# Performance work log

Hardware: AMD Instinct MI355X
Metric: run time of the kernel (lower is better)

Reference implementation:

```python
import jax, jax.numpy as jnp
import numpy as np

NUM_HEADS = 16

def setup_inputs() -> dict:
    key = jax.random.key(0)
    k1, k2, k3 = jax.random.split(key, 3)
    B, T, D = 4, 2048, 1024
    x = jax.random.normal(k1, (B, T, D), dtype=jnp.float32)
    # lecun_normal: std = 1/sqrt(fan_in)
    w = jax.random.normal(k2, (3 * D, D), dtype=jnp.float32) * (1.0 / np.sqrt(D))
    w_out = jax.random.normal(k3, (D, D), dtype=jnp.float32) * (1.0 / np.sqrt(D))
    return {"x": x, "w": w, "w_out": w_out}


def reference(x, w, w_out):
    B, T, D = x.shape
    H = NUM_HEADS
    L = D // H
    # qkv projection: (B,T,3D)
    q, k, v = jnp.split(jnp.matmul(x, w.T), 3, axis=2)
    # -> (T,B,H,L) time-major for the scan
    q = q.reshape(B, T, H, L).transpose(1, 0, 2, 3)
    k = k.reshape(B, T, H, L).transpose(1, 0, 2, 3)
    v = v.reshape(B, T, H, L).transpose(1, 0, 2, 3)
    scale = jax.lax.rsqrt(jnp.float32(L))
    k_exp = jnp.exp(k * scale) + 1e-6            # (T,B,H,L)
    k_norm = jnp.cumsum(k_exp, axis=0)           # causal normalizer
    qs = jax.nn.softmax(q * scale, axis=-1) / k_norm

    def step(carry, args):
        qs_t, k_t, v_t = args                    # each (B,H,L)
        # accumulate outer product k_t v_t^T into (B,H,L,L) state
        carry = carry + k_t[..., :, None] * v_t[..., None, :]
        y_t = jnp.einsum('bhl,bhlm->bhm', qs_t, carry)
        return carry, y_t

    init = jnp.zeros((B, H, L, L), dtype=x.dtype)
    _, y = jax.lax.scan(step, init, (qs, k_exp, v))   # y: (T,B,H,L)
    y = y.reshape(T, B, D).transpose(1, 0, 2)         # (B,T,D)
    return jnp.matmul(y, w_out)                       # Dense, no bias
```

## Files before the change

kernel.cpp:

```cpp
#include <hip/hip_runtime.h>
#include <math.h>

#define Bsz   4
#define Tsz   2048
#define Dsz   1024
#define Hsz   16
#define Lsz   64
#define BHsz  64
#define CH    64
#define NCH   32
#define QKVLD 3072
#define SCL   0.125f
#define QSC   512.0f
#define QSCI  (1.0f/512.0f)

typedef float  floatx4 __attribute__((ext_vector_type(4)));
typedef _Float16 half8 __attribute__((ext_vector_type(8)));
typedef _Float16 half4 __attribute__((ext_vector_type(4)));
typedef _Float16 half2v __attribute__((ext_vector_type(2)));

#define AS1 __attribute__((address_space(1)))
#define AS3 __attribute__((address_space(3)))

static __device__ __forceinline__ void gload_lds16(const void* g, void* l) {
  __builtin_amdgcn_global_load_lds((const AS1 unsigned int*)g,
                                   (AS3 unsigned int*)l, 16, 0, 0);
}

static __device__ __forceinline__ float wave_max64(float v) {
#pragma unroll
  for (int off = 1; off < 64; off <<= 1) v = fmaxf(v, __shfl_xor(v, off));
  return v;
}
static __device__ __forceinline__ float wave_sum64(float v) {
#pragma unroll
  for (int off = 1; off < 64; off <<= 1) v += __shfl_xor(v, off);
  return v;
}

__launch_bounds__(256)
__global__ void prep(const float* __restrict__ x, _Float16* __restrict__ xh,
                     const float* __restrict__ w, _Float16* __restrict__ wh,
                     const float* __restrict__ wo, _Float16* __restrict__ woT) {
  const int blk = blockIdx.x, tid = threadIdx.x;
  if (blk < 11264) {
    const float* in  = (blk < 8192) ? x : w;
    _Float16*   outp = (blk < 8192) ? xh : wh;
    const int bi = (blk < 8192) ? blk : blk - 8192;
    const int i = (bi * 256 + tid) * 4;
    float4 v = *(const float4*)(in + i);
    half4 h = { (_Float16)v.x, (_Float16)v.y, (_Float16)v.z, (_Float16)v.w };
    *(half4*)(outp + i) = h;
  } else {
    __shared__ float tile[32][33];
    const int bi = blk - 11264;
    const int bx = (bi & 31) * 32;
    const int by = (bi >> 5) * 32;
    const int tx = tid & 31, ty0 = tid >> 5;
#pragma unroll
    for (int p = 0; p < 4; p++) {
      const int ty = ty0 + p * 8;
      tile[ty][tx] = wo[(size_t)(by + ty) * 1024 + bx + tx];
    }
    __syncthreads();
#pragma unroll
    for (int p = 0; p < 4; p++) {
      const int ty = ty0 + p * 8;
      woT[(size_t)(bx + ty) * 1024 + by + tx] = (_Float16)tile[tx][ty];
    }
  }
}

__launch_bounds__(512, 2)
__global__ void qkv_gemm8(const _Float16* __restrict__ A, const _Float16* __restrict__ B,
                          _Float16* __restrict__ C) {
  __shared__ __align__(16) _Float16 AsF[2 * 256 * 64];
  __shared__ __align__(16) _Float16 BsF[2 * 256 * 64];
  const int tid  = threadIdx.x;
  const int wv   = tid >> 6, lane = tid & 63;
  const int wm   = wv >> 2, wn = wv & 3;
  const int fr   = lane & 15, fq = lane >> 4;

  const int flat = blockIdx.x;
  const int g  = (flat & 7) * 48 + (flat >> 3);
  const int m0 = (g / 12) * 256;
  const int n0 = (g % 12) * 256;

  const int srow = lane >> 3;
  const int scg  = (lane & 7) ^ srow;
  const int wv8  = wv * 8;
  const _Float16* aSrc = A + (size_t)(m0 + wv8 + srow) * 1024 + scg * 8;
  const _Float16* bSrc = B + (size_t)(n0 + wv8 + srow) * 1024 + scg * 8;

  const int sw  = fr & 7;
  const int ck0 = ((0 + fq) ^ sw) * 8;
  const int ck1 = ((4 + fq) ^ sw) * 8;
  const _Float16* apt = AsF + (wm * 64 + fr) * 64;
  const _Float16* bpt = BsF + (wn * 32 + fr) * 64;

  floatx4 acc[8][4];
#pragma unroll
  for (int i = 0; i < 8; i++)
#pragma unroll
    for (int j = 0; j < 4; j++) acc[i][j] = (floatx4){0.f, 0.f, 0.f, 0.f};

  half8 aF[8];
  half8 bF0[4], bF1[4];

#define BAR2() do { __builtin_amdgcn_s_barrier();                              \
                    asm volatile("" ::: "memory"); } while (0)
#define VMW4() asm volatile("s_waitcnt vmcnt(4)" ::: "memory")
#define SYNC() do { __builtin_amdgcn_s_barrier();                              \
    asm volatile("s_waitcnt lgkmcnt(0)" ::: "memory");                         \
    __builtin_amdgcn_sched_barrier(0); } while (0)

#define STAGE_A(kt, hm, sbuf) do {                                             \
    const _Float16* s_ = aSrc + (hm) * (128 * 1024) + (kt) * 64;               \
    gload_lds16(s_,             &AsF[(sbuf) * 16384 + ((hm) * 128 + wv8) * 64]);      \
    gload_lds16(s_ + 64 * 1024, &AsF[(sbuf) * 16384 + ((hm) * 128 + 64 + wv8) * 64]); \
  } while (0)
#define STAGE_B(kt, hm, sbuf) do {                                             \
    const _Float16* s_ = bSrc + (hm) * (128 * 1024) + (kt) * 64;               \
    gload_lds16(s_,             &BsF[(sbuf) * 16384 + ((hm) * 128 + wv8) * 64]);      \
    gload_lds16(s_ + 64 * 1024, &BsF[(sbuf) * 16384 + ((hm) * 128 + 64 + wv8) * 64]); \
  } while (0)

#define RD_A(buf, qm) do {                                                     \
    _Pragma("unroll")                                                          \
    for (int mf = 0; mf < 4; mf++) {                                           \
      const _Float16* p_ = apt + (buf) * 16384 + (qm) * 8192 + mf * 1024;      \
      aF[mf * 2]     = *(const half8*)(p_ + ck0);                              \
      aF[mf * 2 + 1] = *(const half8*)(p_ + ck1);                              \
    } } while (0)
#define RD_B(buf, qn, dst) do {                                                \
    _Pragma("unroll")                                                          \
    for (int nf = 0; nf < 2; nf++) {                                           \
      const _Float16* p_ = bpt + (buf) * 16384 + (qn) * 8192 + nf * 1024;      \
      dst[nf * 2]     = *(const half8*)(p_ + ck0);                             \
      dst[nf * 2 + 1] = *(const half8*)(p_ + ck1);                             \
    } } while (0)

#define MM(qm, qn, bb) do {                                                    \
    __builtin_amdgcn_s_setprio(1);                                             \
    _Pragma("unroll")                                                          \
    for (int mf = 0; mf < 4; mf++)                                             \
      _Pragma("unroll")                                                        \
      for (int nf = 0; nf < 2; nf++) {                                         \
        acc[(qm) * 4 + mf][(qn) * 2 + nf] = __builtin_amdgcn_mfma_f32_16x16x32_f16( \
            aF[mf * 2], bb[nf * 2], acc[(qm) * 4 + mf][(qn) * 2 + nf], 0, 0, 0);     \
        acc[(qm) * 4 + mf][(qn) * 2 + nf] = __builtin_amdgcn_mfma_f32_16x16x32_f16( \
            aF[mf * 2 + 1], bb[nf * 2 + 1], acc[(qm) * 4 + mf][(qn) * 2 + nf], 0, 0, 0); \
      }                                                                        \
    __builtin_amdgcn_s_setprio(0);                                             \
  } while (0)

  STAGE_A(0, 0, 0); STAGE_B(0, 0, 0); STAGE_A(0, 1, 0); STAGE_B(0, 1, 0);
  STAGE_A(1, 0, 1); STAGE_B(1, 0, 1);
  VMW4(); BAR2();

#pragma unroll 1
  for (int t = 0; t < 16; t += 2) {
    RD_A(0, 0); RD_B(0, 0, bF0); STAGE_A(t + 1, 1, 1);
    SYNC(); MM(0, 0, bF0); BAR2();

    RD_B(0, 1, bF1); STAGE_B(t + 1, 1, 1); STAGE_A(t + 2, 0, 0);
    SYNC(); MM(0, 1, bF1); BAR2();

    RD_A(0, 1); STAGE_B(t + 2, 0, 0);
    SYNC(); MM(1, 1, bF1); BAR2();

    VMW4();
    SYNC(); MM(1, 0, bF0); BAR2();

    RD_A(1, 0); RD_B(1, 0, bF0); STAGE_A(t + 2, 1, 0);
    SYNC(); MM(0, 0, bF0); BAR2();

    RD_B(1, 1, bF1); STAGE_B(t + 2, 1, 0); STAGE_A(t + 3, 0, 1);
    SYNC(); MM(0, 1, bF1); BAR2();

    RD_A(1, 1); STAGE_B(t + 3, 0, 1);
    SYNC(); MM(1, 1, bF1); BAR2();

    VMW4();
    SYNC(); MM(1, 0, bF0); BAR2();
  }

#undef MM
#undef RD_B
#undef RD_A
#undef STAGE_B
#undef STAGE_A
#undef SYNC
#undef VMW4
#undef BAR2

  const bool kreg = (n0 >= 1024) && (n0 < 2048);
#pragma unroll
  for (int qm = 0; qm < 2; qm++)
#pragma unroll
    for (int mf = 0; mf < 4; mf++) {
      const int row = m0 + qm * 128 + wm * 64 + mf * 16 + fq * 4;
#pragma unroll
      for (int qn = 0; qn < 2; qn++)
#pragma unroll
        for (int nf = 0; nf < 2; nf++) {
          const int col = n0 + qn * 128 + wn * 32 + nf * 16 + fr;
#pragma unroll
          for (int r = 0; r < 4; r++) {
            float v = acc[qm * 4 + mf][qn * 2 + nf][r];
            if (kreg) v = __expf(v * SCL) + 1e-6f;
            C[(size_t)(row + r) * 3072 + col] = (_Float16)v;
          }
        }
    }
}

__launch_bounds__(256)
__global__ void gemm2(const _Float16* __restrict__ A, const _Float16* __restrict__ B,
                      float* __restrict__ C) {
  __shared__ __align__(16) _Float16 As[2][128][32];
  __shared__ __align__(16) _Float16 Bs[2][128][32];
  const int tid = threadIdx.x;
  const int wv = tid >> 6, lane = tid & 63;
  const int wm = wv >> 1, wn = wv & 1;
  const int fr = lane & 15, fq = lane >> 4;

  const int flat = blockIdx.x;
  const int xcd = flat & 7, loc = flat >> 3;
  const int m0 = (xcd * 8 + (loc >> 3)) * 128;
  const int n0 = (loc & 7) * 128;

  const int srow = lane >> 2;
  const int scg  = lane & 3;
  const _Float16* aSrc = A + (size_t)(m0 + wv * 32 + srow) * 1024 + scg * 8;
  const _Float16* bSrc = B + (size_t)(n0 + wv * 32 + srow) * 1024 + scg * 8;
  _Float16* aBase = &As[0][0][0];
  _Float16* bBase = &Bs[0][0][0];

  const _Float16* apt = aBase + (wm * 64 + fr) * 32 + fq * 8;
  const _Float16* bpt = bBase + (wn * 64 + fr) * 32 + fq * 8;

  floatx4 acc[4][4];
#pragma unroll
  for (int i = 0; i < 4; i++)
#pragma unroll
    for (int j = 0; j < 4; j++) acc[i][j] = (floatx4){0.f, 0.f, 0.f, 0.f};

  half8 aF[4], bF[4];

#define BAR2() do { __builtin_amdgcn_s_barrier();                              \
                    asm volatile("" ::: "memory"); } while (0)
#define VMW4() asm volatile("s_waitcnt vmcnt(4)" ::: "memory")
#define SYNC() do { __builtin_amdgcn_s_barrier();                              \
    asm volatile("s_waitcnt lgkmcnt(0)" ::: "memory");                         \
    __builtin_amdgcn_sched_barrier(0); } while (0)

#define STAGE(kt, bufi) do {                                                   \
    const _Float16* sa_ = aSrc + (size_t)(kt) * 32;                            \
    const _Float16* sb_ = bSrc + (size_t)(kt) * 32;                            \
    gload_lds16(sa_,             aBase + (bufi) * 4096 + (wv * 32) * 32 + lane * 8);      \
    gload_lds16(sa_ + 16 * 1024, aBase + (bufi) * 4096 + (wv * 32 + 16) * 32 + lane * 8); \
    gload_lds16(sb_,             bBase + (bufi) * 4096 + (wv * 32) * 32 + lane * 8);      \
    gload_lds16(sb_ + 16 * 1024, bBase + (bufi) * 4096 + (wv * 32 + 16) * 32 + lane * 8); \
  } while (0)

#define RD8(bufi) do {                                                         \
    _Pragma("unroll")                                                          \
    for (int mf = 0; mf < 4; mf++)                                             \
      aF[mf] = *(const half8*)(apt + (bufi) * 4096 + mf * 512);                \
    _Pragma("unroll")                                                          \
    for (int nf = 0; nf < 4; nf++)                                             \
      bF[nf] = *(const half8*)(bpt + (bufi) * 4096 + nf * 512);                \
  } while (0)

#define MM16() do {                                                            \
    __builtin_amdgcn_s_setprio(1);                                             \
    _Pragma("unroll")                                                          \
    for (int mt = 0; mt < 4; mt++)                                             \
      _Pragma("unroll")                                                        \
      for (int nt = 0; nt < 4; nt++)                                           \
        acc[mt][nt] = __builtin_amdgcn_mfma_f32_16x16x32_f16(aF[mt], bF[nt],   \
                                                             acc[mt][nt], 0, 0, 0); \
    __builtin_amdgcn_s_setprio(0);                                             \
  } while (0)

  STAGE(0, 0);
  STAGE(1, 1);
  VMW4(); BAR2();

#pragma unroll 1
  for (int t = 0; t < 32; t += 2) {
    RD8(0);
    SYNC(); MM16(); BAR2();
    STAGE(t + 2, 0);
    VMW4();
    BAR2();

    RD8(1);
    SYNC(); MM16(); BAR2();
    STAGE(t + 3, 1);
    VMW4();
    BAR2();
  }

#undef MM16
#undef RD8
#undef STAGE
#undef SYNC
#undef VMW4
#undef BAR2

#pragma unroll
  for (int mt = 0; mt < 4; mt++) {
    const int row = m0 + wm * 64 + mt * 16 + fq * 4;
#pragma unroll
    for (int nt = 0; nt < 4; nt++) {
      const int col = n0 + wn * 64 + nt * 16 + fr;
#pragma unroll
      for (int r = 0; r < 4; r++)
        C[(size_t)(row + r) * 1024 + col] = acc[mt][nt][r];
    }
  }
}

__launch_bounds__(256)
__global__ void chunk_kv(const _Float16* __restrict__ qkv, float* __restrict__ KV,
                         float* __restrict__ Ksum) {
  const int blk = blockIdx.x;
  const int bh = blk >> 3, cgrp = blk & 7;
  const int b = bh >> 4, h = bh & 15;
  const int tid = threadIdx.x;
  const int wave = tid >> 6, lane = tid & 63;
  const int fr = lane & 15, fq = lane >> 4;
  const int m2  = (tid & 31) * 2;
  const int tg8 = (tid >> 5) * 8;

  __shared__ __align__(16) _Float16 KxT[64][72];
  __shared__ __align__(16) _Float16 VT [64][72];

  for (int cc = 0; cc < 4; cc++) {
    const int c = cgrp * 4 + cc;
    const size_t base = ((size_t)(b * Tsz + c * CH)) * QKVLD + h * 64;
    __syncthreads();
    half8 klo, khi, vlo, vhi;
#pragma unroll
    for (int j = 0; j < 8; j++) {
      const int t = tg8 + j;
      half2v kk = *(const half2v*)(qkv + base + (size_t)t * QKVLD + 1024 + m2);
      klo[j] = kk[0]; khi[j] = kk[1];
      half2v vv = *(const half2v*)(qkv + base + (size_t)t * QKVLD + 2048 + m2);
      vlo[j] = vv[0]; vhi[j] = vv[1];
    }
    *(half8*)&KxT[m2][tg8]     = klo;
    *(half8*)&KxT[m2 + 1][tg8] = khi;
    *(half8*)&VT[m2][tg8]      = vlo;
    *(half8*)&VT[m2 + 1][tg8]  = vhi;
    __syncthreads();

    floatx4 acc[4];
#pragma unroll
    for (int j = 0; j < 4; j++) acc[j] = (floatx4){0.f, 0.f, 0.f, 0.f};
#pragma unroll
    for (int ks = 0; ks < 2; ks++) {
      half8 av = *(const half8*)&VT[wave * 16 + fr][ks * 32 + fq * 8];
#pragma unroll
      for (int j = 0; j < 4; j++) {
        half8 bv = *(const half8*)&KxT[j * 16 + fr][ks * 32 + fq * 8];
        acc[j] = __builtin_amdgcn_mfma_f32_16x16x32_f16(av, bv, acc[j], 0, 0, 0);
      }
    }
    float* KVp = KV + ((size_t)(bh * NCH + c)) * 4096;
#pragma unroll
    for (int j = 0; j < 4; j++)
#pragma unroll
      for (int r = 0; r < 4; r++)
        KVp[(wave * 16 + fq * 4 + r) * 64 + j * 16 + fr] = acc[j][r];

    if (tid < 64) {
      float s = 0.f;
      const half8* row = (const half8*)&KxT[tid][0];
#pragma unroll
      for (int j8 = 0; j8 < 8; j8++) {
        half8 v8 = row[j8];
#pragma unroll
        for (int j = 0; j < 8; j++) s += (float)v8[j];
      }
      Ksum[(bh * NCH + c) * 64 + tid] = s;
    }
  }
}

__launch_bounds__(256)
__global__ void prefix_kern(float* __restrict__ KV, float* __restrict__ Ksum) {
  const int tid = threadIdx.x;
  if (blockIdx.x < 256) {
    const int bh = blockIdx.x >> 2;
    const int e  = (blockIdx.x & 3) * 1024 + tid * 4;
    float4* p = (float4*)(KV + (size_t)bh * NCH * 4096 + e);
    float4 acc = {0.f, 0.f, 0.f, 0.f};
#pragma unroll 4
    for (int c = 0; c < NCH; c++) {
      float4 t = p[(size_t)c * 1024];
      p[(size_t)c * 1024] = acc;
      acc.x += t.x; acc.y += t.y; acc.z += t.z; acc.w += t.w;
    }
  } else {
    const int cid = (blockIdx.x - 256) * 256 + tid;
    const int bh = cid >> 4, l4 = cid & 15;
    float4* p = (float4*)(Ksum + (size_t)bh * NCH * 64) + l4;
    float4 acc = {0.f, 0.f, 0.f, 0.f};
#pragma unroll 4
    for (int c = 0; c < NCH; c++) {
      float4 t = p[c * 16];
      p[c * 16] = acc;
      acc.x += t.x; acc.y += t.y; acc.z += t.z; acc.w += t.w;
    }
  }
}

__launch_bounds__(256)
__global__ void chunk_y(const _Float16* __restrict__ qkv, const float* __restrict__ KV,
                        const float* __restrict__ Ksum, _Float16* __restrict__ Y) {
  const int bh = blockIdx.x, c = blockIdx.y;
  const int b = bh >> 4, h = bh & 15;
  const int tid = threadIdx.x;
  const int wave = tid >> 6, lane = tid & 63;
  const int fr = lane & 15, fq = lane >> 4;

  __shared__ __align__(16) _Float16 kxh[64][72];
  __shared__ __align__(16) _Float16 kxT[64][72];
  __shared__ __align__(16) _Float16 Ph[64][136];
  __shared__ __align__(16) _Float16 Bh[64][136];

  const size_t base = ((size_t)(b * Tsz + c * CH)) * QKVLD + h * 64;
  const float* KVp = KV + ((size_t)(bh * NCH + c)) * 4096;
  const int ksoff = (bh * NCH + c) * 64;

  _Float16 qreg[16];
#pragma unroll
  for (int i = 0; i < 16; i++)
    qreg[i] = qkv[base + (size_t)(wave * 16 + i) * QKVLD + lane];

  float ksb[4];
#pragma unroll
  for (int j = 0; j < 4; j++) ksb[j] = Ksum[ksoff + j * 16 + fr];

  {
    const int rr  = tid >> 3;
    const int sg8 = (tid & 7) * 8;
#pragma unroll
    for (int p = 0; p < 2; p++) {
      const int t = p * 32 + rr;
      *(half8*)&kxh[t][sg8] =
          *(const half8*)(qkv + base + (size_t)t * QKVLD + 1024 + sg8);
      *(half8*)&Ph[t][64 + sg8] =
          *(const half8*)(qkv + base + (size_t)t * QKVLD + 2048 + sg8);
    }
  }
  {
    const int m  = tid >> 2;
    const int l0 = (tid & 3) * 16;
#pragma unroll
    for (int q = 0; q < 2; q++) {
      float4 s0 = *(const float4*)(KVp + m * 64 + l0 + q * 8);
      float4 s1 = *(const float4*)(KVp + m * 64 + l0 + q * 8 + 4);
      half8 hh = { (_Float16)s0.x, (_Float16)s0.y, (_Float16)s0.z, (_Float16)s0.w,
                   (_Float16)s1.x, (_Float16)s1.y, (_Float16)s1.z, (_Float16)s1.w };
      *(half8*)&Bh[m][l0 + q * 8] = hh;
    }
  }
  __syncthreads();

  {
    const int l2  = (tid & 31) * 2;
    const int tg8 = (tid >> 5) * 8;
    half8 k0, k1, v0, v1;
#pragma unroll
    for (int j = 0; j < 8; j++) {
      const int t = tg8 + j;
      half2v kk = *(const half2v*)&kxh[t][l2];
      k0[j] = kk[0]; k1[j] = kk[1];
      half2v vv = *(const half2v*)&Ph[t][64 + l2];
      v0[j] = vv[0]; v1[j] = vv[1];
    }
    *(half8*)&kxT[l2][tg8]          = k0;
    *(half8*)&kxT[l2 + 1][tg8]      = k1;
    *(half8*)&Bh[l2][64 + tg8]      = v0;
    *(half8*)&Bh[l2 + 1][64 + tg8]  = v1;
  }
  __syncthreads();

  {
    floatx4 kacc[4];
#pragma unroll
    for (int j = 0; j < 4; j++) kacc[j] = (floatx4){0.f, 0.f, 0.f, 0.f};
#pragma unroll
    for (int ks = 0; ks < 2; ks++) {
      half8 af;
#pragma unroll
      for (int j = 0; j < 8; j++)
        af[j] = (ks * 32 + fq * 8 + j) <= (wave * 16 + fr) ? (_Float16)1.0f
                                                           : (_Float16)0.0f;
#pragma unroll
      for (int j = 0; j < 4; j++) {
        half8 bf = *(const half8*)&kxT[j * 16 + fr][ks * 32 + fq * 8];
        kacc[j] = __builtin_amdgcn_mfma_f32_16x16x32_f16(af, bf, kacc[j], 0, 0, 0);
      }
    }
    __syncthreads();
#pragma unroll
    for (int j = 0; j < 4; j++)
#pragma unroll
      for (int r = 0; r < 4; r++)
        kxT[wave * 16 + fq * 4 + r][j * 16 + fr] =
            (_Float16)(QSC / (ksb[j] + kacc[j][r]));
  }

#pragma unroll
  for (int i = 0; i < 16; i++) {
    const int t = wave * 16 + i;
    float v = (float)qreg[i] * SCL;
    float m = wave_max64(v);
    float e = __expf(v - m);
    float s = wave_sum64(e);
    Ph[t][lane] = (_Float16)((e / s) * (float)kxT[t][lane]);
  }
  __syncthreads();

  const int wm = (wave >> 1) * 32, wn = (wave & 1) * 32;
  {
    floatx4 a2[2][2];
#pragma unroll
    for (int mt = 0; mt < 2; mt++)
#pragma unroll
      for (int nt = 0; nt < 2; nt++) a2[mt][nt] = (floatx4){0.f, 0.f, 0.f, 0.f};
#pragma unroll
    for (int ks = 0; ks < 2; ks++) {
      half8 af[2], bf[2];
#pragma unroll
      for (int i = 0; i < 2; i++) {
        af[i] = *(const half8*)&Ph[wm + i * 16 + fr][ks * 32 + fq * 8];
        bf[i] = *(const half8*)&kxh[wn + i * 16 + fr][ks * 32 + fq * 8];
      }
#pragma unroll
      for (int mt = 0; mt < 2; mt++)
#pragma unroll
        for (int nt = 0; nt < 2; nt++)
          a2[mt][nt] = __builtin_amdgcn_mfma_f32_16x16x32_f16(af[mt], bf[nt], a2[mt][nt], 0, 0, 0);
    }
#pragma unroll
    for (int mt = 0; mt < 2; mt++)
#pragma unroll
      for (int nt = 0; nt < 2; nt++)
#pragma unroll
        for (int r = 0; r < 4; r++) {
          const int t = wm + mt * 16 + fq * 4 + r;
          const int s = wn + nt * 16 + fr;
          Ph[t][64 + s] = (_Float16)(s <= t ? a2[mt][nt][r] : 0.f);
        }
  }
  __syncthreads();

  {
    floatx4 acc[2][2];
#pragma unroll
    for (int mt = 0; mt < 2; mt++)
#pragma unroll
      for (int nt = 0; nt < 2; nt++) acc[mt][nt] = (floatx4){0.f, 0.f, 0.f, 0.f};
#pragma unroll
    for (int ks = 0; ks < 4; ks++) {
      half8 af[2], bf[2];
#pragma unroll
      for (int i = 0; i < 2; i++) {
        af[i] = *(const half8*)&Ph[wm + i * 16 + fr][ks * 32 + fq * 8];
        bf[i] = *(const half8*)&Bh[wn + i * 16 + fr][ks * 32 + fq * 8];
      }
#pragma unroll
      for (int mt = 0; mt < 2; mt++)
#pragma unroll
        for (int nt = 0; nt < 2; nt++)
          acc[mt][nt] = __builtin_amdgcn_mfma_f32_16x16x32_f16(af[mt], bf[nt], acc[mt][nt], 0, 0, 0);
    }
#pragma unroll
    for (int mt = 0; mt < 2; mt++)
#pragma unroll
      for (int nt = 0; nt < 2; nt++)
#pragma unroll
        for (int r = 0; r < 4; r++)
          kxh[wm + mt * 16 + fq * 4 + r][wn + nt * 16 + fr] =
              (_Float16)(acc[mt][nt][r] * QSCI);
  }
  __syncthreads();

  {
    const int ty = tid >> 2, sg = (tid & 3) * 16;
    _Float16* yrow = Y + (size_t)(b * Tsz + c * CH + ty) * Dsz + h * 64 + sg;
    *(half8*)(yrow)     = *(const half8*)&kxh[ty][sg];
    *(half8*)(yrow + 8) = *(const half8*)&kxh[ty][sg + 8];
  }
}

extern "C" void kernel_launch(void* const* d_in, const int* in_sizes, int n_in,
                              void* d_out, int out_size, void* d_ws, size_t ws_size,
                              hipStream_t stream) {
  const float* x     = (const float*)d_in[0];
  const float* w     = (const float*)d_in[1];
  const float* w_out = (const float*)d_in[2];
  float* out = (float*)d_out;

  _Float16* xh   = (_Float16*)d_ws;
  _Float16* Yh   = xh;
  _Float16* wh   = xh + (size_t)8192 * 1024;
  _Float16* woT  = wh + (size_t)3072 * 1024;
  _Float16* qkvh = woT + (size_t)1024 * 1024;
  float* KV   = (float*)(qkvh + (size_t)8192 * 3072);
  float* Ksum = KV + (size_t)BHsz * NCH * 4096;

  prep<<<12288, 256, 0, stream>>>(x, xh, w, wh, w_out, woT);

  qkv_gemm8<<<384, 512, 0, stream>>>(xh, wh, qkvh);

  chunk_kv<<<512, 256, 0, stream>>>(qkvh, KV, Ksum);
  prefix_kern<<<260, 256, 0, stream>>>(KV, Ksum);
  chunk_y<<<dim3(BHsz, NCH), 256, 0, stream>>>(qkvh, KV, Ksum, Yh);

  gemm2<<<512, 256, 0, stream>>>(Yh, woT, out);
}
```

Measured before the change: 243.7 us.

## Retile QKV GEMM to 128x256 blocks with simple double buffering; drop softmax max

The QKV projection GEMM moves from 256x256 tiles with an eight-phase interleaved load/compute schedule to 128x256 tiles. Each block now issues one combined A/B stage per k-step into two LDS buffers, and each wave computes a 64x64 sub-tile. The grid doubles to 768 blocks, which gives more parallelism and lower register and LDS use, but loses some operand reuse and the finer overlap of the old schedule. Separately, the per-row softmax in chunk_y no longer subtracts the wave-wide max, saving a shuffle reduction. That is safe only while q*scale stays small enough not to overflow exp.

```diff
diff --git a/kernel.cpp b/kernel.cpp
--- a/kernel.cpp
+++ b/kernel.cpp
@@ -27,11 +27,6 @@
                                    (AS3 unsigned int*)l, 16, 0, 0);
 }
 
-static __device__ __forceinline__ float wave_max64(float v) {
-#pragma unroll
-  for (int off = 1; off < 64; off <<= 1) v = fmaxf(v, __shfl_xor(v, off));
-  return v;
-}
 static __device__ __forceinline__ float wave_sum64(float v) {
 #pragma unroll
   for (int off = 1; off < 64; off <<= 1) v += __shfl_xor(v, off);
@@ -72,18 +67,18 @@
 }
 
 __launch_bounds__(512, 2)
-__global__ void qkv_gemm8(const _Float16* __restrict__ A, const _Float16* __restrict__ B,
-                          _Float16* __restrict__ C) {
-  __shared__ __align__(16) _Float16 AsF[2 * 256 * 64];
-  __shared__ __align__(16) _Float16 BsF[2 * 256 * 64];
+__global__ void qkv_gemm(const _Float16* __restrict__ A, const _Float16* __restrict__ B,
+                         _Float16* __restrict__ C) {
+  __shared__ __align__(16) _Float16 As[2 * 128 * 64];
+  __shared__ __align__(16) _Float16 Bs[2 * 256 * 64];
   const int tid  = threadIdx.x;
   const int wv   = tid >> 6, lane = tid & 63;
   const int wm   = wv >> 2, wn = wv & 3;
   const int fr   = lane & 15, fq = lane >> 4;
 
   const int flat = blockIdx.x;
-  const int g  = (flat & 7) * 48 + (flat >> 3);
-  const int m0 = (g / 12) * 256;
+  const int g  = (flat & 7) * 96 + (flat >> 3);
+  const int m0 = (g / 12) * 128;
   const int n0 = (g % 12) * 256;
 
   const int srow = lane >> 3;
@@ -91,128 +86,110 @@
   const int wv8  = wv * 8;
   const _Float16* aSrc = A + (size_t)(m0 + wv8 + srow) * 1024 + scg * 8;
   const _Float16* bSrc = B + (size_t)(n0 + wv8 + srow) * 1024 + scg * 8;
+  _Float16* aBase = &As[0];
+  _Float16* bBase = &Bs[0];
 
   const int sw  = fr & 7;
   const int ck0 = ((0 + fq) ^ sw) * 8;
   const int ck1 = ((4 + fq) ^ sw) * 8;
-  const _Float16* apt = AsF + (wm * 64 + fr) * 64;
-  const _Float16* bpt = BsF + (wn * 32 + fr) * 64;
-
-  floatx4 acc[8][4];
-#pragma unroll
-  for (int i = 0; i < 8; i++)
+  const _Float16* apt = aBase + (wm * 64 + fr) * 64;
+  const _Float16* bpt = bBase + (wn * 64 + fr) * 64;
+
+  floatx4 acc[4][4];
+#pragma unroll
+  for (int i = 0; i < 4; i++)
 #pragma unroll
     for (int j = 0; j < 4; j++) acc[i][j] = (floatx4){0.f, 0.f, 0.f, 0.f};
 
-  half8 aF[8];
-  half8 bF0[4], bF1[4];
+  half8 aF[8], bF[8];
 
 #define BAR2() do { __builtin_amdgcn_s_barrier();                              \
                     asm volatile("" ::: "memory"); } while (0)
-#define VMW4() asm volatile("s_waitcnt vmcnt(4)" ::: "memory")
+#define VMW6() asm volatile("s_waitcnt vmcnt(6)" ::: "memory")
 #define SYNC() do { __builtin_amdgcn_s_barrier();                              \
     asm volatile("s_waitcnt lgkmcnt(0)" ::: "memory");                         \
     __builtin_amdgcn_sched_barrier(0); } while (0)
 
-#define STAGE_A(kt, hm, sbuf) do {                                             \
-    const _Float16* s_ = aSrc + (hm) * (128 * 1024) + (kt) * 64;               \
-    gload_lds16(s_,             &AsF[(sbuf) * 16384 + ((hm) * 128 + wv8) * 64]);      \
-    gload_lds16(s_ + 64 * 1024, &AsF[(sbuf) * 16384 + ((hm) * 128 + 64 + wv8) * 64]); \
+#define STAGE(kt, bufi) do {                                                   \
+    const _Float16* sa_ = aSrc + (size_t)(kt) * 64;                            \
+    const _Float16* sb_ = bSrc + (size_t)(kt) * 64;                            \
+    gload_lds16(sa_,              aBase + (bufi) * 8192  + (wv8) * 64);        \
+    gload_lds16(sa_ + 64 * 1024,  aBase + (bufi) * 8192  + (64 + wv8) * 64);   \
+    gload_lds16(sb_,              bBase + (bufi) * 16384 + (wv8) * 64);        \
+    gload_lds16(sb_ + 64 * 1024,  bBase + (bufi) * 16384 + (64 + wv8) * 64);   \
+    gload_lds16(sb_ + 128 * 1024, bBase + (bufi) * 16384 + (128 + wv8) * 64);  \
+    gload_lds16(sb_ + 192 * 1024, bBase + (bufi) * 16384 + (192 + wv8) * 64);  \
   } while (0)
-#define STAGE_B(kt, hm, sbuf) do {                                             \
-    const _Float16* s_ = bSrc + (hm) * (128 * 1024) + (kt) * 64;               \
-    gload_lds16(s_,             &BsF[(sbuf) * 16384 + ((hm) * 128 + wv8) * 64]);      \
-    gload_lds16(s_ + 64 * 1024, &BsF[(sbuf) * 16384 + ((hm) * 128 + 64 + wv8) * 64]); \
-  } while (0)
-
-#define RD_A(buf, qm) do {                                                     \
+
+#define RD16(bufi) do {                                                        \
     _Pragma("unroll")                                                          \
     for (int mf = 0; mf < 4; mf++) {                                           \
-      const _Float16* p_ = apt + (buf) * 16384 + (qm) * 8192 + mf * 1024;      \
+      const _Float16* p_ = apt + (bufi) * 8192 + mf * 1024;                    \
       aF[mf * 2]     = *(const half8*)(p_ + ck0);                              \
       aF[mf * 2 + 1] = *(const half8*)(p_ + ck1);                              \
+    }                                                                          \
+    _Pragma("unroll")                                                          \
+    for (int nf = 0; nf < 4; nf++) {                                           \
+      const _Float16* p_ = bpt + (bufi) * 16384 + nf * 1024;                   \
+      bF[nf * 2]     = *(const half8*)(p_ + ck0);                              \
+      bF[nf * 2 + 1] = *(const half8*)(p_ + ck1);                              \
     } } while (0)
-#define RD_B(buf, qn, dst) do {                                                \
-    _Pragma("unroll")                                                          \
-    for (int nf = 0; nf < 2; nf++) {                                           \
-      const _Float16* p_ = bpt + (buf) * 16384 + (qn) * 8192 + nf * 1024;      \
-      dst[nf * 2]     = *(const half8*)(p_ + ck0);                             \
-      dst[nf * 2 + 1] = *(const half8*)(p_ + ck1);                             \
-    } } while (0)
-
-#define MM(qm, qn, bb) do {                                                    \
+
+#define MM32() do {                                                            \
     __builtin_amdgcn_s_setprio(1);                                             \
     _Pragma("unroll")                                                          \
-    for (int mf = 0; mf < 4; mf++)                                             \
+    for (int mt = 0; mt < 4; mt++)                                             \
       _Pragma("unroll")                                                        \
-      for (int nf = 0; nf < 2; nf++) {                                         \
-        acc[(qm) * 4 + mf][(qn) * 2 + nf] = __builtin_amdgcn_mfma_f32_16x16x32_f16( \
-            aF[mf * 2], bb[nf * 2], acc[(qm) * 4 + mf][(qn) * 2 + nf], 0, 0, 0);     \
-        acc[(qm) * 4 + mf][(qn) * 2 + nf] = __builtin_amdgcn_mfma_f32_16x16x32_f16( \
-            aF[mf * 2 + 1], bb[nf * 2 + 1], acc[(qm) * 4 + mf][(qn) * 2 + nf], 0, 0, 0); \
+      for (int nt = 0; nt < 4; nt++) {                                         \
+        acc[mt][nt] = __builtin_amdgcn_mfma_f32_16x16x32_f16(                  \
+            aF[mt * 2], bF[nt * 2], acc[mt][nt], 0, 0, 0);                     \
+        acc[mt][nt] = __builtin_amdgcn_mfma_f32_16x16x32_f16(                  \
+            aF[mt * 2 + 1], bF[nt * 2 + 1], acc[mt][nt], 0, 0, 0);             \
       }                                                                        \
     __builtin_amdgcn_s_setprio(0);                                             \
   } while (0)
 
-  STAGE_A(0, 0, 0); STAGE_B(0, 0, 0); STAGE_A(0, 1, 0); STAGE_B(0, 1, 0);
-  STAGE_A(1, 0, 1); STAGE_B(1, 0, 1);
-  VMW4(); BAR2();
+  STAGE(0, 0);
+  STAGE(1, 1);
+  VMW6(); BAR2();
 
 #pragma unroll 1
   for (int t = 0; t < 16; t += 2) {
-    RD_A(0, 0); RD_B(0, 0, bF0); STAGE_A(t + 1, 1, 1);
-    SYNC(); MM(0, 0, bF0); BAR2();
-
-    RD_B(0, 1, bF1); STAGE_B(t + 1, 1, 1); STAGE_A(t + 2, 0, 0);
-    SYNC(); MM(0, 1, bF1); BAR2();
-
-    RD_A(0, 1); STAGE_B(t + 2, 0, 0);
-    SYNC(); MM(1, 1, bF1); BAR2();
-
-    VMW4();
-    SYNC(); MM(1, 0, bF0); BAR2();
-
-    RD_A(1, 0); RD_B(1, 0, bF0); STAGE_A(t + 2, 1, 0);
-    SYNC(); MM(0, 0, bF0); BAR2();
-
-    RD_B(1, 1, bF1); STAGE_B(t + 2, 1, 0); STAGE_A(t + 3, 0, 1);
-    SYNC(); MM(0, 1, bF1); BAR2();
-
-    RD_A(1, 1); STAGE_B(t + 3, 0, 1);
-    SYNC(); MM(1, 1, bF1); BAR2();
-
-    VMW4();
-    SYNC(); MM(1, 0, bF0); BAR2();
-  }
-
-#undef MM
-#undef RD_B
-#undef RD_A
-#undef STAGE_B
-#undef STAGE_A
+    RD16(0);
+    SYNC(); MM32(); BAR2();
+    STAGE(t + 2, 0);
+    VMW6();
+    BAR2();
+
+    RD16(1);
+    SYNC(); MM32(); BAR2();
+    STAGE(t + 3, 1);
+    VMW6();
+    BAR2();
+  }
+
+#undef MM32
+#undef RD16
+#undef STAGE
 #undef SYNC
-#undef VMW4
+#undef VMW6
 #undef BAR2
 
   const bool kreg = (n0 >= 1024) && (n0 < 2048);
 #pragma unroll
-  for (int qm = 0; qm < 2; qm++)
-#pragma unroll
-    for (int mf = 0; mf < 4; mf++) {
-      const int row = m0 + qm * 128 + wm * 64 + mf * 16 + fq * 4;
-#pragma unroll
-      for (int qn = 0; qn < 2; qn++)
-#pragma unroll
-        for (int nf = 0; nf < 2; nf++) {
-          const int col = n0 + qn * 128 + wn * 32 + nf * 16 + fr;
-#pragma unroll
-          for (int r = 0; r < 4; r++) {
-            float v = acc[qm * 4 + mf][qn * 2 + nf][r];
-            if (kreg) v = __expf(v * SCL) + 1e-6f;
-            C[(size_t)(row + r) * 3072 + col] = (_Float16)v;
-          }
-        }
-    }
+  for (int mt = 0; mt < 4; mt++) {
+    const int row = m0 + wm * 64 + mt * 16 + fq * 4;
+#pragma unroll
+    for (int nt = 0; nt < 4; nt++) {
+      const int col = n0 + wn * 64 + nt * 16 + fr;
+#pragma unroll
+      for (int r = 0; r < 4; r++) {
+        float v = acc[mt][nt][r];
+        if (kreg) v = __expf(v * SCL) + 1e-6f;
+        C[(size_t)(row + r) * 3072 + col] = (_Float16)v;
+      }
+    }
+  }
 }
 
 __launch_bounds__(256)
@@ -519,9 +496,7 @@
 #pragma unroll
   for (int i = 0; i < 16; i++) {
     const int t = wave * 16 + i;
-    float v = (float)qreg[i] * SCL;
-    float m = wave_max64(v);
-    float e = __expf(v - m);
+    float e = __expf((float)qreg[i] * SCL);
     float s = wave_sum64(e);
     Ph[t][lane] = (_Float16)((e / s) * (float)kxT[t][lane]);
   }
@@ -618,7 +593,7 @@
 
   prep<<<12288, 256, 0, stream>>>(x, xh, w, wh, w_out, woT);
 
-  qkv_gemm8<<<384, 512, 0, stream>>>(xh, wh, qkvh);
+  qkv_gemm<<<768, 512, 0, stream>>>(xh, wh, qkvh);
 
   chunk_kv<<<512, 256, 0, stream>>>(qkvh, KV, Ksum);
   prefix_kern<<<260, 256, 0, stream>>>(KV, Ksum);
```

Measured after the change: 240.1 us. About the same (-1.5%).
